# Optimization experiments

Measured on AMD Instinct MI355X. Metric: run time of the kernel, lower is better.

Reference implementation:

```python
import jax, jax.numpy as jnp
import numpy as np

B, L, D_IN, H = 64, 512, 1024, 1024

def setup_inputs() -> dict:
    key = jax.random.key(0)
    k1, k2, k3 = jax.random.split(key, 3)
    x = jax.random.normal(k1, (B, L, D_IN), dtype=jnp.float32)
    # nn.Linear(input_sz + hidden_dim, 4*hidden_dim): weight [4H, H + D_IN], bias [4H]
    # concat order in forward is (hidden_state, input_at_t)
    W = jax.random.normal(k2, (4 * H, H + D_IN), dtype=jnp.float32) * 0.02
    b = jax.random.normal(k3, (4 * H,), dtype=jnp.float32) * 0.02
    return {"x": x, "W": W, "b": b}

def reference(x, W, b):
    Bsz = x.shape[0]
    Hd = W.shape[0] // 4
    # split weight into hidden part and input part (concat order: [h, x_t])
    Wh = W[:, :Hd]          # [4H, H]
    Wx = W[:, Hd:]          # [4H, D_IN]
    # precompute input projections for all timesteps: [B, L, 4H]
    x_proj = jnp.einsum('bld,gd->blg', x, Wx) + b
    h0 = jnp.zeros((Bsz, Hd), dtype=x.dtype)
    c0 = jnp.zeros((Bsz, Hd), dtype=x.dtype)

    def step(carry, xp_t):
        h, c = carry
        gates = xp_t + h @ Wh.T                     # [B, 4H]
        f_l, i_l, g_l, o_l = jnp.split(gates, 4, axis=-1)
        f = jax.nn.sigmoid(f_l)
        i = jax.nn.sigmoid(i_l)
        g = jnp.tanh(g_l)
        o = jax.nn.sigmoid(o_l)
        c_new = f * c + i * g
        h_new = o * jnp.tanh(c_new)
        return (h_new, c_new), h_new

    (h_fin, c_fin), hs = jax.lax.scan(step, (h0, c0), jnp.swapaxes(x_proj, 0, 1))
    outputs = jnp.swapaxes(hs, 0, 1)  # [B, L, H]
    return outputs, (h_fin, c_fin)
```

## Files before the change

### kernel.cpp

```cpp
#include <hip/hip_runtime.h>
#include <hip/hip_bf16.h>
#include <stdint.h>

#define B_SZ   64
#define L_SEQ  512
#define DIN    1024
#define HDIM   1024
#define OUT_HFIN 33554432L
#define OUT_CFIN 33619968L

typedef float  f32x4 __attribute__((ext_vector_type(4)));
typedef short  s16x8 __attribute__((ext_vector_type(8)));
typedef unsigned short u16;
typedef unsigned int   u32;
typedef unsigned long long u64;

#define OFF_XBF   0ULL
#define OFF_WX    67108864ULL
#define OFF_MB    67108864ULL
#define OFF_WH    75497472ULL
#define OFF_XPROJ 83886080ULL

static __device__ __forceinline__ u16 f2bf(float f) {
    __hip_bfloat16 h = __float2bfloat16(f);
    return *reinterpret_cast<u16*>(&h);
}
static __device__ __forceinline__ float bf2f(u16 u) {
    union { uint32_t i; float f; } v;
    v.i = ((uint32_t)u) << 16;
    return v.f;
}
static __device__ __forceinline__ float fsigmoid(float x) {
    return __builtin_amdgcn_rcpf(1.0f + __expf(-x));
}
static __device__ __forceinline__ float ftanh(float x) {
    return 1.0f - 2.0f * __builtin_amdgcn_rcpf(1.0f + __expf(2.0f * x));
}
static __device__ __forceinline__ void gload_lds16(const u16* g, u16* l) {
    __builtin_amdgcn_global_load_lds((const __attribute__((address_space(1))) void*)g,
                                     (__attribute__((address_space(3))) void*)l, 16, 0, 0);
}

__global__ void prep_kernel(const float* __restrict__ x, const float* __restrict__ W,
                            u16* __restrict__ xbf, u16* __restrict__ wx,
                            u16* __restrict__ wh) {
    long tid = (long)blockIdx.x * blockDim.x + threadIdx.x;
    long stride = (long)gridDim.x * blockDim.x;
    const long NX4 = 33554432 / 4;
    for (long i = tid; i < NX4; i += stride) {
        float4 v = ((const float4*)x)[i];
        ushort4 o;
        o.x = f2bf(v.x); o.y = f2bf(v.y); o.z = f2bf(v.z); o.w = f2bf(v.w);
        ((ushort4*)xbf)[i] = o;
    }
    const long NW4 = 8388608 / 4;
    for (long i = tid; i < NW4; i += stride) {
        float4 v = ((const float4*)W)[i];
        long f = i * 4;
        long n = f >> 11;
        long c = f & 2047;
        ushort4 o;
        o.x = f2bf(v.x); o.y = f2bf(v.y); o.z = f2bf(v.z); o.w = f2bf(v.w);
        u16* dst = (c < 1024) ? &wh[n * 1024 + c] : &wx[n * 1024 + (c - 1024)];
        *(ushort4*)dst = o;
    }
}

__global__ void mbzero_kernel(float4* __restrict__ mb) {
    int i = blockIdx.x * blockDim.x + threadIdx.x;
    mb[i] = make_float4(0.f, 0.f, 0.f, 0.f);
}

__global__ __launch_bounds__(256) void xproj_gemm(const u16* __restrict__ xbf,
                                                  const u16* __restrict__ wxbf,
                                                  const float* __restrict__ bias,
                                                  u16* __restrict__ xproj) {
    __shared__ u16 As[2][128 * 32];
    __shared__ u16 Bs[2][128 * 32];
    const int tid  = threadIdx.x;
    const int lane = tid & 63;
    const int w    = tid >> 6;
    const int wm   = w >> 1, wn = w & 1;
    const int l15  = lane & 15, quad = lane >> 4;
    const int m0 = blockIdx.y * 128;
    const int n0 = blockIdx.x * 128;

    const u16* ga = xbf  + (long)(m0 + (tid >> 2)) * 1024 + (tid & 3) * 8;
    const u16* gb = wxbf + (long)(n0 + (tid >> 2)) * 1024 + (tid & 3) * 8;

    f32x4 acc[4][4];
#pragma unroll
    for (int i = 0; i < 4; ++i)
#pragma unroll
        for (int j = 0; j < 4; ++j) acc[i][j] = 0.0f;

#define STAGE(buf, k0)                                                    \
    do {                                                                  \
        gload_lds16(ga + (k0),         &As[buf][w * 512]);                \
        gload_lds16(ga + 65536 + (k0), &As[buf][2048 + w * 512]);         \
        gload_lds16(gb + (k0),         &Bs[buf][w * 512]);                \
        gload_lds16(gb + 65536 + (k0), &Bs[buf][2048 + w * 512]);         \
    } while (0)

    STAGE(0, 0);
    __syncthreads();

    for (int kt = 0; kt < 32; ++kt) {
        const int cur = kt & 1;
        if (kt < 31) STAGE(cur ^ 1, (kt + 1) * 32);

        s16x8 af[4], bfr[4];
#pragma unroll
        for (int mt = 0; mt < 4; ++mt)
            af[mt] = *(const s16x8*)&As[cur][(wm * 64 + mt * 16 + l15) * 32 + quad * 8];
#pragma unroll
        for (int nt = 0; nt < 4; ++nt)
            bfr[nt] = *(const s16x8*)&Bs[cur][(wn * 64 + nt * 16 + l15) * 32 + quad * 8];
#pragma unroll
        for (int mt = 0; mt < 4; ++mt)
#pragma unroll
            for (int nt = 0; nt < 4; ++nt)
                acc[mt][nt] = __builtin_amdgcn_mfma_f32_16x16x32_bf16(af[mt], bfr[nt], acc[mt][nt], 0, 0, 0);

        __syncthreads();
    }
#undef STAGE

#pragma unroll
    for (int nt = 0; nt < 4; ++nt) {
        int n = n0 + wn * 64 + nt * 16 + l15;
        float bv = bias[n];
#pragma unroll
        for (int mt = 0; mt < 4; ++mt) {
            int mbase = m0 + wm * 64 + mt * 16 + quad * 4;
#pragma unroll
            for (int r = 0; r < 4; ++r)
                xproj[(long)(mbase + r) * 4096 + n] = f2bf(acc[mt][nt][r] + bv);
        }
    }
}

__global__ __launch_bounds__(256, 1) void lstm_rec(const u16* __restrict__ whbf,
                                                   const u16* __restrict__ xproj,
                                                   u64* __restrict__ mbbuf,
                                                   float* __restrict__ out) {
    __shared__ __align__(16) u16 h_sw[4][16][272];
    __shared__ float part[2][4][16][4][17];

    const int tid  = threadIdx.x;
    const int w    = tid >> 6;
    const int lane = tid & 63;
    const int l15  = lane & 15, quad = lane >> 4;
    const int g    = blockIdx.x & 3;
    const int jc   = blockIdx.x >> 2;
    const int bbase = g * 16;
    const int crow = 4 * w + quad;
    const int ccol = l15;

    s16x8 bfrag[4][8];
#pragma unroll
    for (int gate = 0; gate < 4; ++gate) {
        const long nrow = (long)gate * 1024 + jc * 16 + l15;
#pragma unroll
        for (int kc = 0; kc < 8; ++kc)
            bfrag[gate][kc] = *(const s16x8*)&whbf[nrow * 1024 + w * 256 + kc * 32 + quad * 8];
    }

    float c_reg = 0.0f;
    const u64* mbrd0 = mbbuf + (u64)g * 8192 + w * 128 + lane;
    u64* mbwr0 = mbbuf + (u64)g * 8192 + (u64)crow * 512 + jc * 8 + (l15 >> 1);

    const u16* xpcell = xproj + (long)(bbase + crow) * 512 * 4096 + jc * 16 + ccol;
    float xp[4];
#pragma unroll
    for (int gate = 0; gate < 4; ++gate)
        xp[gate] = bf2f(xpcell[(long)gate * 1024]);

    for (int t = 0; t < 512; ++t) {
        if (t == 0) {
#pragma unroll
            for (int i = 0; i < 32; ++i)
                *(u32*)&h_sw[w][i >> 1][((i & 1) * 64 + lane) * 2] = 0u;
        } else {
            const u64* mbr = mbrd0 + ((t + 1) & 1) * 32768;
            u64 tmp[32];
            for (;;) {
#pragma unroll
                for (int i = 0; i < 32; ++i)
                    tmp[i] = __hip_atomic_load(&mbr[(i >> 1) * 512 + (i & 1) * 64],
                                               __ATOMIC_RELAXED, __HIP_MEMORY_SCOPE_AGENT);
                u32 bad = 0;
#pragma unroll
                for (int i = 0; i < 32; ++i)
                    bad |= ((u32)(tmp[i] >> 32)) ^ (u32)t;
                if (__ballot(bad != 0) == 0ULL) break;
            }
#pragma unroll
            for (int i = 0; i < 32; ++i)
                *(u32*)&h_sw[w][i >> 1][((i & 1) * 64 + lane) * 2] = (u32)tmp[i];
        }

        f32x4 acc[4];
#pragma unroll
        for (int gate = 0; gate < 4; ++gate) acc[gate] = 0.0f;
#pragma unroll
        for (int kc = 0; kc < 8; ++kc) {
            s16x8 a = *(const s16x8*)&h_sw[w][l15][kc * 32 + quad * 8];
            acc[0] = __builtin_amdgcn_mfma_f32_16x16x32_bf16(a, bfrag[0][kc], acc[0], 0, 0, 0);
            acc[1] = __builtin_amdgcn_mfma_f32_16x16x32_bf16(a, bfrag[1][kc], acc[1], 0, 0, 0);
            acc[2] = __builtin_amdgcn_mfma_f32_16x16x32_bf16(a, bfrag[2][kc], acc[2], 0, 0, 0);
            acc[3] = __builtin_amdgcn_mfma_f32_16x16x32_bf16(a, bfrag[3][kc], acc[3], 0, 0, 0);
        }
#pragma unroll
        for (int gate = 0; gate < 4; ++gate)
#pragma unroll
            for (int r = 0; r < 4; ++r)
                part[t & 1][gate][quad * 4 + r][w][l15] = acc[gate][r];
        __syncthreads();

        float gv[4];
#pragma unroll
        for (int gate = 0; gate < 4; ++gate) {
            float p0 = part[t & 1][gate][crow][0][ccol];
            float p1 = part[t & 1][gate][crow][1][ccol];
            float p2 = part[t & 1][gate][crow][2][ccol];
            float p3 = part[t & 1][gate][crow][3][ccol];
            gv[gate] = ((p0 + p1) + (p2 + p3)) + xp[gate];
        }
        float fv = fsigmoid(gv[0]);
        float iv = fsigmoid(gv[1]);
        float gg = ftanh   (gv[2]);
        float ov = fsigmoid(gv[3]);
        c_reg = fv * c_reg + iv * gg;
        float h = ov * ftanh(c_reg);

        if (t < 511) {
            float hn = __shfl_xor(h, 1);
            if ((l15 & 1) == 0) {
                u32 data = (u32)f2bf(h) | ((u32)f2bf(hn) << 16);
                u64 slot = ((u64)(u32)(t + 1) << 32) | (u64)data;
                __hip_atomic_store(mbwr0 + (t & 1) * 32768, slot,
                                   __ATOMIC_RELAXED, __HIP_MEMORY_SCOPE_AGENT);
            }
        }

        long bg = bbase + crow;
        long j  = jc * 16 + ccol;
        out[(bg * 512 + t) * 1024 + j] = h;
        if (t == 511) {
            out[OUT_HFIN + bg * 1024 + j] = h;
            out[OUT_CFIN + bg * 1024 + j] = c_reg;
        } else {
#pragma unroll
            for (int gate = 0; gate < 4; ++gate)
                xp[gate] = bf2f(xpcell[((long)t + 1) * 4096 + (long)gate * 1024]);
        }
    }
}

extern "C" void kernel_launch(void* const* d_in, const int* in_sizes, int n_in,
                              void* d_out, int out_size, void* d_ws, size_t ws_size,
                              hipStream_t stream) {
    const float* x    = (const float*)d_in[0];
    const float* W    = (const float*)d_in[1];
    const float* bias = (const float*)d_in[2];
    float* out = (float*)d_out;
    char*  ws  = (char*)d_ws;

    u16* xbf   = (u16*)(ws + OFF_XBF);
    u16* wx    = (u16*)(ws + OFF_WX);
    u16* wh    = (u16*)(ws + OFF_WH);
    u16* xproj = (u16*)(ws + OFF_XPROJ);
    u64* mb    = (u64*)(ws + OFF_MB);

    hipLaunchKernelGGL(prep_kernel, dim3(2048), dim3(256), 0, stream, x, W, xbf, wx, wh);
    hipLaunchKernelGGL(xproj_gemm, dim3(32, 256), dim3(256), 0, stream, xbf, wx, bias, xproj);
    hipLaunchKernelGGL(mbzero_kernel, dim3(128), dim3(256), 0, stream, (float4*)mb);
    hipLaunchKernelGGL(lstm_rec, dim3(256), dim3(256), 0, stream, wh, xproj, mb, out);
}
```

Baseline: 2.089 ms.

## Load recurrent h directly into MFMA fragment layout, skipping LDS staging

Changes the mailbox layout so each lane's atomic loads already hold its MFMA A-operand fragment. The h_sw shared-memory round trip (store then reload) is removed. Polling now re-reads only the slots that are still stale instead of all 32. The next timestep's x-projection load is issued at the top of the step so it overlaps the spin-wait. This adds register pressure and changes the writer-side address pattern, which may be less coalesced.

```diff
diff --git a/kernel.cpp b/kernel.cpp
--- a/kernel.cpp
+++ b/kernel.cpp
@@ -144,7 +144,6 @@
                                                    const u16* __restrict__ xproj,
                                                    u64* __restrict__ mbbuf,
                                                    float* __restrict__ out) {
-    __shared__ __align__(16) u16 h_sw[4][16][272];
     __shared__ float part[2][4][16][4][17];
 
     const int tid  = threadIdx.x;
@@ -167,37 +166,48 @@
     }
 
     float c_reg = 0.0f;
-    const u64* mbrd0 = mbbuf + (u64)g * 8192 + w * 128 + lane;
-    u64* mbwr0 = mbbuf + (u64)g * 8192 + (u64)crow * 512 + jc * 8 + (l15 >> 1);
+    const u64* mbrd0 = mbbuf + (u64)g * 8192 + w * 2048 + quad * 64 + l15;
+    u64* mbwr0 = mbbuf + (u64)g * 8192 + jc * 128 + (l15 >> 1) * 16 + 4 * w + quad;
 
     const u16* xpcell = xproj + (long)(bbase + crow) * 512 * 4096 + jc * 16 + ccol;
-    float xp[4];
+    float xp[4], xpn[4];
 #pragma unroll
     for (int gate = 0; gate < 4; ++gate)
         xp[gate] = bf2f(xpcell[(long)gate * 1024]);
 
     for (int t = 0; t < 512; ++t) {
+        if (t < 511) {
+#pragma unroll
+            for (int gate = 0; gate < 4; ++gate)
+                xpn[gate] = bf2f(xpcell[((long)t + 1) * 4096 + (long)gate * 1024]);
+        }
+
+        u64 tmp[32];
         if (t == 0) {
 #pragma unroll
-            for (int i = 0; i < 32; ++i)
-                *(u32*)&h_sw[w][i >> 1][((i & 1) * 64 + lane) * 2] = 0u;
+            for (int i = 0; i < 32; ++i) tmp[i] = 0ULL;
         } else {
             const u64* mbr = mbrd0 + ((t + 1) & 1) * 32768;
-            u64 tmp[32];
-            for (;;) {
+#pragma unroll
+            for (int i = 0; i < 32; ++i)
+                tmp[i] = __hip_atomic_load(&mbr[(i >> 2) * 256 + (i & 3) * 16],
+                                           __ATOMIC_RELAXED, __HIP_MEMORY_SCOPE_AGENT);
+            u32 bm = 0;
+#pragma unroll
+            for (int i = 0; i < 32; ++i)
+                bm |= ((u32)(tmp[i] >> 32) != (u32)t) ? (1u << i) : 0u;
+            while (__ballot(bm != 0) != 0ULL) {
 #pragma unroll
                 for (int i = 0; i < 32; ++i)
-                    tmp[i] = __hip_atomic_load(&mbr[(i >> 1) * 512 + (i & 1) * 64],
-                                               __ATOMIC_RELAXED, __HIP_MEMORY_SCOPE_AGENT);
-                u32 bad = 0;
+                    if (bm & (1u << i))
+                        tmp[i] = __hip_atomic_load(&mbr[(i >> 2) * 256 + (i & 3) * 16],
+                                                   __ATOMIC_RELAXED, __HIP_MEMORY_SCOPE_AGENT);
+                u32 nbm = 0;
 #pragma unroll
                 for (int i = 0; i < 32; ++i)
-                    bad |= ((u32)(tmp[i] >> 32)) ^ (u32)t;
-                if (__ballot(bad != 0) == 0ULL) break;
+                    nbm |= ((u32)(tmp[i] >> 32) != (u32)t) ? (1u << i) : 0u;
+                bm = nbm;
             }
-#pragma unroll
-            for (int i = 0; i < 32; ++i)
-                *(u32*)&h_sw[w][i >> 1][((i & 1) * 64 + lane) * 2] = (u32)tmp[i];
         }
 
         f32x4 acc[4];
@@ -205,11 +215,15 @@
         for (int gate = 0; gate < 4; ++gate) acc[gate] = 0.0f;
 #pragma unroll
         for (int kc = 0; kc < 8; ++kc) {
-            s16x8 a = *(const s16x8*)&h_sw[w][l15][kc * 32 + quad * 8];
-            acc[0] = __builtin_amdgcn_mfma_f32_16x16x32_bf16(a, bfrag[0][kc], acc[0], 0, 0, 0);
-            acc[1] = __builtin_amdgcn_mfma_f32_16x16x32_bf16(a, bfrag[1][kc], acc[1], 0, 0, 0);
-            acc[2] = __builtin_amdgcn_mfma_f32_16x16x32_bf16(a, bfrag[2][kc], acc[2], 0, 0, 0);
-            acc[3] = __builtin_amdgcn_mfma_f32_16x16x32_bf16(a, bfrag[3][kc], acc[3], 0, 0, 0);
+            union { u32 u[4]; s16x8 v; } a;
+            a.u[0] = (u32)tmp[kc * 4 + 0];
+            a.u[1] = (u32)tmp[kc * 4 + 1];
+            a.u[2] = (u32)tmp[kc * 4 + 2];
+            a.u[3] = (u32)tmp[kc * 4 + 3];
+            acc[0] = __builtin_amdgcn_mfma_f32_16x16x32_bf16(a.v, bfrag[0][kc], acc[0], 0, 0, 0);
+            acc[1] = __builtin_amdgcn_mfma_f32_16x16x32_bf16(a.v, bfrag[1][kc], acc[1], 0, 0, 0);
+            acc[2] = __builtin_amdgcn_mfma_f32_16x16x32_bf16(a.v, bfrag[2][kc], acc[2], 0, 0, 0);
+            acc[3] = __builtin_amdgcn_mfma_f32_16x16x32_bf16(a.v, bfrag[3][kc], acc[3], 0, 0, 0);
         }
 #pragma unroll
         for (int gate = 0; gate < 4; ++gate)
@@ -250,11 +264,9 @@
         if (t == 511) {
             out[OUT_HFIN + bg * 1024 + j] = h;
             out[OUT_CFIN + bg * 1024 + j] = c_reg;
-        } else {
-#pragma unroll
-            for (int gate = 0; gate < 4; ++gate)
-                xp[gate] = bf2f(xpcell[((long)t + 1) * 4096 + (long)gate * 1024]);
-        }
+        }
+#pragma unroll
+        for (int gate = 0; gate < 4; ++gate) xp[gate] = xpn[gate];
     }
 }
 
```

After: 2.849 ms. +36.4%, slower.
